# Optimization experiments

Measured on AMD Instinct MI355X. Metric: run time of the kernel, lower is better.

The kernel has to match this reference:

```python
import jax, jax.numpy as jnp
import numpy as np

# Fixed model constants from setParams()
TAU_W, TAU_N, TAU_R = 1.5e6, 6.0e5, 6.0e4
TAU_E, TAU_G, TAU_A = 2.5e4, 1.0e4, 1.0e4
F_W_MAX, F_N_MAX, F_R_MAX = 6.5, 5.0, 5.0
ALPHA_W, ALPHA_N, ALPHA_R = 0.5, 0.175, 0.13
BETA_W, BETA_R = -0.4, -0.9
GAMMA_E, GAMMA_G, GAMMA_A = 5.0, 4.0, 2.0
H_MAX, THETA_W = 1.0, 2.0
TAU_HW, TAU_HS = 3.483e7, 3.06e7
KAPPA = 1.5
A_RK = (0.5, 0.5, 1.0, 1.0)

T, B = 10000, 512


def setup_inputs() -> dict:
    key = jax.random.key(0)
    noise = 0.05 * jax.random.normal(key, (T, B), dtype=jnp.float32)
    return {
        "noise_input": noise,
        "g_RRe": jnp.float32(1.3),
        "g_RWe": jnp.float32(1.6),
        "g_WNi": jnp.float32(-2.0),
        "g_WRi": jnp.float32(-4.0),
        "g_NRi": jnp.float32(-1.3),
        "g_NWi": jnp.float32(-1.68),
    }


def _heaviside(x):
    # smooth heaviside: sigmoid with steepness 5
    return jax.nn.sigmoid(5.0 * x)


def reference(noise_input, g_RRe, g_RWe, g_WNi, g_WRi, g_NRi, g_NWi):
    b = noise_input.shape[1]
    dt = noise_input.dtype
    init = (
        jnp.full((b,), 6.0, dt),    # f_W
        jnp.full((b,), 1e-3, dt),   # f_N
        jnp.full((b,), 1e-3, dt),   # f_R
        jnp.full((b,), 0.9, dt),    # c_WXi
        jnp.full((b,), 1e-3, dt),   # c_NXi
        jnp.full((b,), 1e-3, dt),   # c_RXe
        jnp.full((b,), 0.5, dt),    # h
    )

    def step(state, noise):
        fW0, fN0, fR0, cW0, cN0, cR0, h0 = state
        # RK moment lists; index 0 is the step's initial value
        fW = [fW0]; fN = [fN0]; fR = [fR0]
        cW = [cW0]; cN = [cN0]; cR = [cR0]; hh = [h0]
        for n in range(4):
            a = A_RK[n]
            I_W = g_NWi * cN[n] + g_RWe * cR[n] + noise
            I_N = g_WNi * cW[n] + noise
            I_R = g_WRi * cW[n] + g_NRi * cN[n] + g_RRe * cR[n] + noise
            fW.append(fW[0] + a * (F_W_MAX * 0.5 * (1.0 + jnp.tanh((I_W - BETA_W) / ALPHA_W)) - fW[n]) / TAU_W)
            fN.append(fN[0] + a * (F_N_MAX * 0.5 * (1.0 + jnp.tanh((I_N + KAPPA * hh[n]) / ALPHA_N)) - fN[n]) / TAU_N)
            fR.append(fR[0] + a * (F_R_MAX * 0.5 * (1.0 + jnp.tanh((I_R - BETA_R) / ALPHA_R)) - fR[n]) / TAU_R)
            cW.append(cW[0] + a * (jnp.tanh(fW[n + 1] / GAMMA_E) - cW[n]) / TAU_E)
            cN.append(cN[0] + a * (jnp.tanh(fN[n + 1] / GAMMA_G) - cN[n]) / TAU_G)
            cR.append(cR[0] + a * (jnp.tanh(fR[n + 1] / GAMMA_A) - cR[n]) / TAU_A)
            hh.append(hh[0] + a * ((H_MAX - hh[n]) / TAU_HW * _heaviside(fW[n] - THETA_W)
                                   - hh[n] / TAU_HS * _heaviside(THETA_W - fW[n])))
        comb = lambda v: (-3.0 * v[0] + 2.0 * v[1] + 4.0 * v[2] + 2.0 * v[3] + v[4]) / 6.0
        new_state = tuple(comb(v) for v in (fW, fN, fR, cW, cN, cR, hh))
        return new_state, jnp.stack(new_state)  # [7, B]

    _, traj = jax.lax.scan(step, init, noise_input)
    return traj  # [T, 7, B]
```

## Files before the change

### kernel.cpp

```cpp
#include <hip/hip_runtime.h>

#define T_STEPS 10000
#define BATCH   512

__device__ __forceinline__ float fexp2(float x) {
#if __has_builtin(__builtin_amdgcn_exp2f)
  return __builtin_amdgcn_exp2f(x);
#else
  return exp2f(x);
#endif
}

__device__ __forceinline__ float frcp(float x) {
#if __has_builtin(__builtin_amdgcn_rcpf)
  return __builtin_amdgcn_rcpf(x);
#else
  return 1.0f / x;
#endif
}

#define PIN(x) asm volatile("" : "+v"(x))

template <int CTRL>
__device__ __forceinline__ float qperm(float v) {
  int i = __builtin_bit_cast(int, v);
#if __has_builtin(__builtin_amdgcn_mov_dpp)
  int r = __builtin_amdgcn_mov_dpp(i, CTRL, 0xF, 0xF, true);
#else
  int r = __builtin_amdgcn_ds_swizzle(i, 0x8000 | CTRL);
#endif
  return __builtin_bit_cast(float, r);
}

__global__ __launch_bounds__(64, 1)
void sleep_rk4_kernel(const float* __restrict__ noise,
                      const float* __restrict__ pgRRe,
                      const float* __restrict__ pgRWe,
                      const float* __restrict__ pgWNi,
                      const float* __restrict__ pgWRi,
                      const float* __restrict__ pgNRi,
                      const float* __restrict__ pgNWi,
                      float* __restrict__ out)
{
  __shared__ float shm[16 * 128];

  const int tid  = (int)(blockIdx.x * 64u + threadIdx.x);
  const int b    = tid >> 2;
  const int bl   = b & 15;
  const int role = tid & 3;

  const float g_RRe = *pgRRe, g_RWe = *pgRWe, g_WNi = *pgWNi;
  const float g_WRi = *pgWRi, g_NRi = *pgNRi, g_NWi = *pgNWi;

  const float L2E = 1.4426950408889634f;
  const float LN2 = 0.6931471805599453f;

  float W1, W2, W3, NSC, BB, qa, qb, pa, pb, cs, ia, ib;
  float f0, c0;
  bool role03;

  if (role == 0) {
    const float SC = 2.0f * L2E / 0.5f;
    W1 = SC * g_NWi; W2 = SC * g_RWe; W3 = 0.0f; NSC = SC; BB = SC * 0.4f;
    qa = -1.0f / 1.5e6f; qb = 6.5f / 1.5e6f; pa = 0.0f; pb = -6.5f / 1.5e6f;
    cs = 2.0f * L2E / 5.0f; ia = -1.0f / 2.5e4f; ib = 1.0f / 2.5e4f;
    f0 = 6.0f; c0 = 0.9f; role03 = true;
  } else if (role == 1) {
    const float SC = 2.0f * L2E / 0.175f;
    W1 = SC * g_WNi; W2 = SC * 1.5f; W3 = 0.0f; NSC = SC; BB = 0.0f;
    qa = -1.0f / 6.0e5f; qb = 5.0f / 6.0e5f; pa = 0.0f; pb = -5.0f / 6.0e5f;
    cs = 2.0f * L2E / 4.0f; ia = -1.0f / 1.0e4f; ib = 1.0f / 1.0e4f;
    f0 = 1.0e-3f; c0 = 1.0e-3f; role03 = false;
  } else if (role == 2) {
    const float SC = 2.0f * L2E / 0.13f;
    W1 = SC * g_WRi; W2 = SC * g_NRi; W3 = SC * g_RRe; NSC = SC; BB = SC * 0.9f;
    qa = -1.0f / 6.0e4f; qb = 5.0f / 6.0e4f; pa = 0.0f; pb = -5.0f / 6.0e4f;
    cs = 2.0f * L2E / 2.0f; ia = -1.0f / 1.0e4f; ib = 1.0f / 1.0e4f;
    f0 = 1.0e-3f; c0 = 1.0e-3f; role03 = false;
  } else {
    W1 = 0.0f; W2 = -5.0f * L2E; W3 = 0.0f; NSC = 0.0f; BB = 10.0f * L2E;
    qa = -1.0f / 3.06e7f; qb = 0.0f;
    pa = (1.0f / 3.06e7f - 1.0f / 3.483e7f);
    pb = 1.0f / 3.483e7f;
    cs = 0.0f; ia = 0.0f; ib = 0.0f;
    f0 = 0.5f; c0 = 0.0f; role03 = true;
  }

  const float AQAh = 0.5f * qa, AQA1 = qa;
  const float AIAh = 0.5f * ia, AIA1 = ia;
  const float IAC  = ia * cs;
  const float TIA  = 2.0f * ia;
  const float R6   = 0.16666666666666666f;

  float vF[4], vG[4];
  auto frun = [&](float f0b, float Gb, float* v) -> float {
    const float Chb = fmaf(0.5f, Gb, f0b), C1b = f0b + Gb;
    float s0 = f0b, acc = -3.0f * f0b;
    s0 = fmaf(AQAh, s0, Chb); v[0] = s0; acc = fmaf(2.0f, s0, acc);
    s0 = fmaf(AQAh, s0, Chb); v[1] = s0; acc = fmaf(4.0f, s0, acc);
    s0 = fmaf(AQA1, s0, C1b); v[2] = s0; acc = fmaf(2.0f, s0, acc);
    s0 = fmaf(AQA1, s0, C1b); v[3] = s0; acc = fmaf(1.0f, s0, acc);
    float q = acc * R6; q = fmaf(fmaf(q, -6.0f, acc), R6, q); return q;
  };
  const float KF = frun(1.0f, 0.0f, vF);
  const float KG = frun(0.0f, 1.0f, vG);

  auto crun = [&](const float* v, float c0b, float e1u, float vd1) -> float {
    const float E1h = IAC * e1u, E11 = 2.0f * IAC * e1u;
    const float Dh = c0b + 0.5f * vd1, D1 = c0b + vd1;
    float s1 = c0b, acc = -3.0f * c0b;
    s1 = fmaf(AIAh, s1, fmaf(E1h, v[0], Dh)); acc = fmaf(2.0f, s1, acc);
    s1 = fmaf(AIAh, s1, fmaf(E1h, v[1], Dh)); acc = fmaf(4.0f, s1, acc);
    s1 = fmaf(AIA1, s1, fmaf(E11, v[2], D1)); acc = fmaf(2.0f, s1, acc);
    s1 = fmaf(AIA1, s1, fmaf(E11, v[3], D1)); acc = fmaf(1.0f, s1, acc);
    float q = acc * R6; q = fmaf(fmaf(q, -6.0f, acc), R6, q); return q;
  };
  float z4[4] = {0.0f, 0.0f, 0.0f, 0.0f};
  const float KC  = crun(z4, 1.0f, 0.0f, 0.0f);
  const float LAf = crun(vF, 0.0f, 1.0f, 0.0f);
  const float LBf = crun(vG, 0.0f, 1.0f, 0.0f);
  const float KW  = crun(z4, 0.0f, 0.0f, 1.0f);

  const float KGi  = 1.0f / KG;
  const float LBfK = LBf * KGi;
  const float qbK  = qb * KG;

  float LAe, LBK, VDK, PK, tLAe, tLBK, tVDK, tPK;
  auto crefresh_compute = [&](float fcur) {
    const float zb = cs * fcur;
    const float ez = fexp2(zb);
    const float sc_ = frcp(1.0f + ez);
    const float t2 = fmaf(sc_, sc_, -sc_);
    const float e1 = LN2 * t2;
    const float vC = fmaf(-e1, zb, sc_);
    const float VD1 = fmaf(TIA, vC, ib);
    tLAe = LAf * e1; tLBK = LBfK * e1; tVDK = KW * VD1;
    tPK = fmaf(pa, fcur, pb) * KG;
  };
  crefresh_compute(f0);
  LAe = tLAe; LBK = tLBK; VDK = tVDK; PK = tPK;

  float dF = 0.0f, dC = 0.0f;
  float Gq0, Gq1, Gq2, Gq3, Gq4, Gq5, Gq6, Gq7;

  const int offA = role * 16 + bl;
  const int offB = (role + 4) * 16 + bl;

  const int  L        = (int)threadIdx.x;
  const bool fluseful = ((L & 31) < 28);
  float* gp;
  {
    const int p  = L & 31;
    const int rg = p >> 2;
    const int v  = (rg == 3) ? 6 : ((rg < 3) ? rg : (rg > 6 ? 0 : rg - 1));
    gp = out + (L >> 5) * 3584 + v * 512 + (p & 3) * 4 + (int)(blockIdx.x * 16u);
  }

  float nbA[16], nbB[16], nbCv[16];
#pragma unroll
  for (int j = 0; j < 16; ++j) nbA[j] = noise[b + j * BATCH];
#pragma unroll
  for (int j = 0; j < 16; ++j) nbB[j] = noise[b + (16 + j) * BATCH];

  {
    const float pubS = role03 ? f0 : c0;
    const float xAs = qperm<0x01>(c0);
    const float xBs = qperm<0x1E>(pubS);
    const float YB = fmaf(W1, xAs, fmaf(W2, xBs, fmaf(W3, c0, BB)));
    Gq0 = fmaf(PK, frcp(1.0f + fexp2(fmaf(NSC, nbA[0], YB))), qbK);
    Gq1 = fmaf(PK, frcp(1.0f + fexp2(fmaf(NSC, nbA[1], YB))), qbK);
    Gq2 = fmaf(PK, frcp(1.0f + fexp2(fmaf(NSC, nbA[2], YB))), qbK);
    Gq3 = fmaf(PK, frcp(1.0f + fexp2(fmaf(NSC, nbA[3], YB))), qbK);
    Gq4 = fmaf(PK, frcp(1.0f + fexp2(fmaf(NSC, nbA[4], YB))), qbK);
    Gq5 = fmaf(PK, frcp(1.0f + fexp2(fmaf(NSC, nbA[5], YB))), qbK);
    Gq6 = fmaf(PK, frcp(1.0f + fexp2(fmaf(NSC, nbA[6], YB))), qbK);
    Gq7 = fmaf(PK, frcp(1.0f + fexp2(fmaf(NSC, nbA[7], YB))), qbK);
  }

  auto GROUP8 = [&](int SJ, float n0, float n1, float n2, float n3,
                    float n4, float n5, float n6, float n7) {
    const float pubS = role03 ? f0 : c0;
    const float pubD = role03 ? dF : dC;
    const float xAs = qperm<0x01>(c0);
    const float xBs = qperm<0x1E>(pubS);
    const float xAd = qperm<0x01>(dC);
    const float xBd = qperm<0x1E>(pubD);
    float YB = fmaf(W3, c0, BB);
    float dY = W3 * dC;
    const float f1 = fmaf(KF, f0, Gq0);
    const float c1 = fmaf(KC, c0, fmaf(LAe, f0, fmaf(LBK, Gq0, VDK)));
    YB = fmaf(W2, xBs, YB);
    dY = fmaf(W2, xBd, dY);
    const float f2 = fmaf(KF, f1, Gq1);
    const float c2 = fmaf(KC, c1, fmaf(LAe, f1, fmaf(LBK, Gq1, VDK)));
    YB = fmaf(W1, xAs, YB);
    dY = fmaf(W1, xAd, dY);
    const float f3 = fmaf(KF, f2, Gq2);
    const float c3 = fmaf(KC, c2, fmaf(LAe, f2, fmaf(LBK, Gq2, VDK)));
    const float y0 = fmaf(NSC, n0, fmaf( 8.5f, dY, YB));
    const float y1 = fmaf(NSC, n1, fmaf( 9.5f, dY, YB));
    const float y2 = fmaf(NSC, n2, fmaf(10.5f, dY, YB));
    const float y3 = fmaf(NSC, n3, fmaf(11.5f, dY, YB));
    const float f4 = fmaf(KF, f3, Gq3);
    const float c4 = fmaf(KC, c3, fmaf(LAe, f3, fmaf(LBK, Gq3, VDK)));
    const float y4 = fmaf(NSC, n4, fmaf(12.5f, dY, YB));
    const float y5 = fmaf(NSC, n5, fmaf(13.5f, dY, YB));
    const float y6 = fmaf(NSC, n6, fmaf(14.5f, dY, YB));
    const float y7 = fmaf(NSC, n7, fmaf(15.5f, dY, YB));
    const float e0 = fexp2(y0);
    const float e1_ = fexp2(y1);
    const float f5 = fmaf(KF, f4, Gq4);
    const float c5 = fmaf(KC, c4, fmaf(LAe, f4, fmaf(LBK, Gq4, VDK)));
    const float e2 = fexp2(y2);
    const float e3 = fexp2(y3);
    const float f6 = fmaf(KF, f5, Gq5);
    const float c6 = fmaf(KC, c5, fmaf(LAe, f5, fmaf(LBK, Gq5, VDK)));
    const float e4 = fexp2(y4);
    const float e5 = fexp2(y5);
    const float f7 = fmaf(KF, f6, Gq6);
    const float c7 = fmaf(KC, c6, fmaf(LAe, f6, fmaf(LBK, Gq6, VDK)));
    const float e6 = fexp2(y6);
    const float e7 = fexp2(y7);
    const float f8 = fmaf(KF, f7, Gq7);
    const float c8 = fmaf(KC, c7, fmaf(LAe, f7, fmaf(LBK, Gq7, VDK)));
    const float r0 = frcp(1.0f + e0);
    const float r1 = frcp(1.0f + e1_);
    const float r2 = frcp(1.0f + e2);
    const float r3 = frcp(1.0f + e3);
    const float r4 = frcp(1.0f + e4);
    const float r5 = frcp(1.0f + e5);
    const float r6 = frcp(1.0f + e6);
    const float r7 = frcp(1.0f + e7);
    shm[(SJ + 0) * 128 + offA] = f1;  shm[(SJ + 0) * 128 + offB] = c1;
    shm[(SJ + 1) * 128 + offA] = f2;  shm[(SJ + 1) * 128 + offB] = c2;
    shm[(SJ + 2) * 128 + offA] = f3;  shm[(SJ + 2) * 128 + offB] = c3;
    shm[(SJ + 3) * 128 + offA] = f4;  shm[(SJ + 3) * 128 + offB] = c4;
    shm[(SJ + 4) * 128 + offA] = f5;  shm[(SJ + 4) * 128 + offB] = c5;
    shm[(SJ + 5) * 128 + offA] = f6;  shm[(SJ + 5) * 128 + offB] = c6;
    shm[(SJ + 6) * 128 + offA] = f7;  shm[(SJ + 6) * 128 + offB] = c7;
    shm[(SJ + 7) * 128 + offA] = f8;  shm[(SJ + 7) * 128 + offB] = c8;
    Gq0 = fmaf(PK, r0, qbK);
    Gq1 = fmaf(PK, r1, qbK);
    Gq2 = fmaf(PK, r2, qbK);
    Gq3 = fmaf(PK, r3, qbK);
    Gq4 = fmaf(PK, r4, qbK);
    Gq5 = fmaf(PK, r5, qbK);
    Gq6 = fmaf(PK, r6, qbK);
    Gq7 = fmaf(PK, r7, qbK);
    dF = f8 - f7; dC = c8 - c7;
    f0 = f8; c0 = c8;
  };

  int base = 0;

#define TBLOCK(nb1_, nb2_, nbL_)                                              \
  do {                                                                        \
    int tl = base + 32; if (tl > T_STEPS - 16) tl = T_STEPS - 16;             \
    const float* __restrict__ lp = noise + (size_t)tl * BATCH;                \
    _Pragma("unroll")                                                         \
    for (int j = 0; j < 16; ++j) nbL_[j] = lp[b + j * BATCH];                 \
    _Pragma("unroll")                                                         \
    for (int j = 8; j < 16; ++j) PIN(nb1_[j]);                                \
    _Pragma("unroll")                                                         \
    for (int j = 0; j < 8; ++j) PIN(nb2_[j]);                                 \
    crefresh_compute(f0);                                                     \
    GROUP8(0, nb1_[8], nb1_[9], nb1_[10], nb1_[11],                           \
              nb1_[12], nb1_[13], nb1_[14], nb1_[15]);                        \
    LAe = tLAe; LBK = tLBK; VDK = tVDK; PK = tPK;                             \
    GROUP8(8, nb2_[0], nb2_[1], nb2_[2], nb2_[3],                             \
              nb2_[4], nb2_[5], nb2_[6], nb2_[7]);                            \
    if (fluseful) {                                                           \
      _Pragma("unroll")                                                       \
      for (int r = 0; r < 8; ++r) {                                           \
        const float4 vv = *(const float4*)&shm[L * 4 + r * 256];              \
        *(float4*)gp = vv;                                                    \
        gp += 7168;                                                           \
      }                                                                       \
    }                                                                         \
    base += 16;                                                               \
  } while (0)

  for (int kk = 0; kk < 208; ++kk) {
    TBLOCK(nbA, nbB, nbCv);
    TBLOCK(nbB, nbCv, nbA);
    TBLOCK(nbCv, nbA, nbB);
  }
  TBLOCK(nbA, nbB, nbCv);
#undef TBLOCK
}

extern "C" void kernel_launch(void* const* d_in, const int* in_sizes, int n_in,
                              void* d_out, int out_size, void* d_ws, size_t ws_size,
                              hipStream_t stream) {
  const float* noise = (const float*)d_in[0];
  const float* gRRe  = (const float*)d_in[1];
  const float* gRWe  = (const float*)d_in[2];
  const float* gWNi  = (const float*)d_in[3];
  const float* gWRi  = (const float*)d_in[4];
  const float* gNRi  = (const float*)d_in[5];
  const float* gNWi  = (const float*)d_in[6];
  float* out = (float*)d_out;

  sleep_rk4_kernel<<<dim3((BATCH * 4) / 64), dim3(64), 0, stream>>>(
      noise, gRRe, gRWe, gWNi, gWRi, gNRi, gNWi, out);
}
```

Before: 464.7 us.

## Double-buffer shared output staging and defer global stores by one block

Shared staging of the trajectory is split into two ping-pong buffers. Each time block now reads the previous block's staged results into registers before compute, and issues the global float4 stores between the two GROUP8 halves. A tail flush writes the last buffer after the loop. The aim is to hide LDS read latency and global store issue inside the serial recurrence compute rather than serialising them at block end. The cost is more LDS, extra registers for the eight float4 values, and reliance on intra-wave ordering instead of a barrier.

```diff
diff --git a/kernel.cpp b/kernel.cpp
--- a/kernel.cpp
+++ b/kernel.cpp
@@ -20,6 +20,7 @@
 }
 
 #define PIN(x) asm volatile("" : "+v"(x))
+#define MEMFENCE() asm volatile("" ::: "memory")
 
 template <int CTRL>
 __device__ __forceinline__ float qperm(float v) {
@@ -42,7 +43,7 @@
                       const float* __restrict__ pgNWi,
                       float* __restrict__ out)
 {
-  __shared__ float shm[16 * 128];
+  __shared__ float shm[2 * 2048];
 
   const int tid  = (int)(blockIdx.x * 64u + threadIdx.x);
   const int b    = tid >> 2;
@@ -177,7 +178,7 @@
     Gq7 = fmaf(PK, frcp(1.0f + fexp2(fmaf(NSC, nbA[7], YB))), qbK);
   }
 
-  auto GROUP8 = [&](int SJ, float n0, float n1, float n2, float n3,
+  auto GROUP8 = [&](int SB, float n0, float n1, float n2, float n3,
                     float n4, float n5, float n6, float n7) {
     const float pubS = role03 ? f0 : c0;
     const float pubD = role03 ? dF : dC;
@@ -231,14 +232,14 @@
     const float r5 = frcp(1.0f + e5);
     const float r6 = frcp(1.0f + e6);
     const float r7 = frcp(1.0f + e7);
-    shm[(SJ + 0) * 128 + offA] = f1;  shm[(SJ + 0) * 128 + offB] = c1;
-    shm[(SJ + 1) * 128 + offA] = f2;  shm[(SJ + 1) * 128 + offB] = c2;
-    shm[(SJ + 2) * 128 + offA] = f3;  shm[(SJ + 2) * 128 + offB] = c3;
-    shm[(SJ + 3) * 128 + offA] = f4;  shm[(SJ + 3) * 128 + offB] = c4;
-    shm[(SJ + 4) * 128 + offA] = f5;  shm[(SJ + 4) * 128 + offB] = c5;
-    shm[(SJ + 5) * 128 + offA] = f6;  shm[(SJ + 5) * 128 + offB] = c6;
-    shm[(SJ + 6) * 128 + offA] = f7;  shm[(SJ + 6) * 128 + offB] = c7;
-    shm[(SJ + 7) * 128 + offA] = f8;  shm[(SJ + 7) * 128 + offB] = c8;
+    shm[SB + 0 * 128 + offA] = f1;  shm[SB + 0 * 128 + offB] = c1;
+    shm[SB + 1 * 128 + offA] = f2;  shm[SB + 1 * 128 + offB] = c2;
+    shm[SB + 2 * 128 + offA] = f3;  shm[SB + 2 * 128 + offB] = c3;
+    shm[SB + 3 * 128 + offA] = f4;  shm[SB + 3 * 128 + offB] = c4;
+    shm[SB + 4 * 128 + offA] = f5;  shm[SB + 4 * 128 + offB] = c5;
+    shm[SB + 5 * 128 + offA] = f6;  shm[SB + 5 * 128 + offB] = c6;
+    shm[SB + 6 * 128 + offA] = f7;  shm[SB + 6 * 128 + offB] = c7;
+    shm[SB + 7 * 128 + offA] = f8;  shm[SB + 7 * 128 + offB] = c8;
     Gq0 = fmaf(PK, r0, qbK);
     Gq1 = fmaf(PK, r1, qbK);
     Gq2 = fmaf(PK, r2, qbK);
@@ -253,40 +254,54 @@
 
   int base = 0;
 
-#define TBLOCK(nb1_, nb2_, nbL_)                                              \
+#define TBLOCK(nb1_, nb2_, nbL_, PH, FL)                                      \
   do {                                                                        \
     int tl = base + 32; if (tl > T_STEPS - 16) tl = T_STEPS - 16;             \
     const float* __restrict__ lp = noise + (size_t)tl * BATCH;                \
     _Pragma("unroll")                                                         \
     for (int j = 0; j < 16; ++j) nbL_[j] = lp[b + j * BATCH];                 \
+    float4 vv[8];                                                             \
+    if (FL && fluseful) {                                                     \
+      _Pragma("unroll")                                                       \
+      for (int r = 0; r < 8; ++r)                                             \
+        vv[r] = *(const float4*)&shm[(PH ^ 1) * 2048 + L * 4 + r * 256];      \
+    }                                                                         \
+    MEMFENCE();                                                               \
     _Pragma("unroll")                                                         \
     for (int j = 8; j < 16; ++j) PIN(nb1_[j]);                                \
     _Pragma("unroll")                                                         \
     for (int j = 0; j < 8; ++j) PIN(nb2_[j]);                                 \
     crefresh_compute(f0);                                                     \
-    GROUP8(0, nb1_[8], nb1_[9], nb1_[10], nb1_[11],                           \
+    GROUP8((PH) * 2048 + 0, nb1_[8], nb1_[9], nb1_[10], nb1_[11],             \
               nb1_[12], nb1_[13], nb1_[14], nb1_[15]);                        \
     LAe = tLAe; LBK = tLBK; VDK = tVDK; PK = tPK;                             \
-    GROUP8(8, nb2_[0], nb2_[1], nb2_[2], nb2_[3],                             \
+    if (FL && fluseful) {                                                     \
+      _Pragma("unroll")                                                       \
+      for (int r = 0; r < 8; ++r) { *(float4*)gp = vv[r]; gp += 7168; }       \
+    }                                                                         \
+    GROUP8((PH) * 2048 + 1024, nb2_[0], nb2_[1], nb2_[2], nb2_[3],            \
               nb2_[4], nb2_[5], nb2_[6], nb2_[7]);                            \
-    if (fluseful) {                                                           \
-      _Pragma("unroll")                                                       \
-      for (int r = 0; r < 8; ++r) {                                           \
-        const float4 vv = *(const float4*)&shm[L * 4 + r * 256];              \
-        *(float4*)gp = vv;                                                    \
-        gp += 7168;                                                           \
-      }                                                                       \
-    }                                                                         \
     base += 16;                                                               \
   } while (0)
 
-  for (int kk = 0; kk < 208; ++kk) {
-    TBLOCK(nbA, nbB, nbCv);
-    TBLOCK(nbB, nbCv, nbA);
-    TBLOCK(nbCv, nbA, nbB);
-  }
-  TBLOCK(nbA, nbB, nbCv);
+  TBLOCK(nbA, nbB, nbCv, 0, 0);
+  for (int kk = 0; kk < 104; ++kk) {
+    TBLOCK(nbB, nbCv, nbA, 1, 1);
+    TBLOCK(nbCv, nbA, nbB, 0, 1);
+    TBLOCK(nbA, nbB, nbCv, 1, 1);
+    TBLOCK(nbB, nbCv, nbA, 0, 1);
+    TBLOCK(nbCv, nbA, nbB, 1, 1);
+    TBLOCK(nbA, nbB, nbCv, 0, 1);
+  }
 #undef TBLOCK
+  if (fluseful) {
+#pragma unroll
+    for (int r = 0; r < 8; ++r) {
+      const float4 vv = *(const float4*)&shm[0 + L * 4 + r * 256];
+      *(float4*)gp = vv;
+      gp += 7168;
+    }
+  }
 }
 
 extern "C" void kernel_launch(void* const* d_in, const int* in_sizes, int n_in,
```

Result: slower. 640.4 us (+37.8%).
